# Kernel tuning notes

Hardware: AMD Instinct MI355X
Metric: run time of the kernel (lower is better)

The kernel has to match this reference:

```python
import jax, jax.numpy as jnp
import numpy as np

THETA = 10000.0
H, D_NOPE, D_ROPE, D_V = 12, 64, 64, 128
D_MODEL, D_LAT = 768, 128
B, S = 4, 2048


def _rope(x, pos, theta=THETA):
    # x: (B, S, D) with D even; pos: (S,) int. Matches RoPE.forward exactly
    # (interleaved even/odd rotation, freqs over full flattened D).
    D = x.shape[-1]
    inv_freq = 1.0 / theta ** (jnp.arange(0, D, 2, dtype=jnp.float32) / D)
    ang = pos.astype(jnp.float32)[:, None] * inv_freq        # (S, D/2)
    c, s = jnp.cos(ang), jnp.sin(ang)
    xe, xo = x[..., 0::2], x[..., 1::2]
    out = jnp.stack([xe * c - xo * s, xe * s + xo * c], axis=-1)
    return out.reshape(x.shape)


def setup_inputs() -> dict:
    key = jax.random.key(0)
    ks = jax.random.split(key, 12)
    std = 0.02
    inp = {
        'x': jax.random.normal(ks[0], (B, S, D_MODEL), jnp.float32),
        'token_positions': jnp.arange(S, dtype=jnp.int64) if jax.config.jax_enable_x64 else jnp.arange(S, dtype=jnp.int32),
        'W_dkv': jax.random.normal(ks[1], (D_LAT, D_MODEL), jnp.float32) * std,
        'b_dkv': jnp.zeros((D_LAT,), jnp.float32),
        'W_dq': jax.random.normal(ks[2], (D_LAT, D_MODEL), jnp.float32) * std,
        'b_dq': jnp.zeros((D_LAT,), jnp.float32),
        'W_uk_nope': jax.random.normal(ks[3], (H * D_NOPE, D_LAT), jnp.float32) * std,
        'b_uk_nope': jnp.zeros((H * D_NOPE,), jnp.float32),
        'W_uv': jax.random.normal(ks[4], (H * D_V, D_LAT), jnp.float32) * std,
        'b_uv': jnp.zeros((H * D_V,), jnp.float32),
        'W_uq_nope': jax.random.normal(ks[5], (H * D_NOPE, D_LAT), jnp.float32) * std,
        'b_uq_nope': jnp.zeros((H * D_NOPE,), jnp.float32),
        'W_uq_rope': jax.random.normal(ks[6], (H * D_ROPE, D_LAT), jnp.float32) * std,
        'b_uq_rope': jnp.zeros((H * D_ROPE,), jnp.float32),
        'W_uk_rope': jax.random.normal(ks[7], (H * D_ROPE, D_MODEL), jnp.float32) * std,
        'b_uk_rope': jnp.zeros((H * D_ROPE,), jnp.float32),
        'W_o': jax.random.normal(ks[8], (D_MODEL, H * D_V), jnp.float32) * std,
        'b_o': jnp.zeros((D_MODEL,), jnp.float32),
    }
    return inp


def reference(x, token_positions, W_dkv, b_dkv, W_dq, b_dq,
              W_uk_nope, b_uk_nope, W_uv, b_uv, W_uq_nope, b_uq_nope,
              W_uq_rope, b_uq_rope, W_uk_rope, b_uk_rope, W_o, b_o):
    b, s, _ = x.shape
    lin = lambda t, W, bb: t @ W.T + bb
    d_qk = D_NOPE + D_ROPE  # 128

    C_kv = lin(x, W_dkv, b_dkv)               # (B,S,128)
    C_q = lin(x, W_dq, b_dq)                  # (B,S,128)

    q_nope = lin(C_q, W_uq_nope, b_uq_nope)   # (B,S,H*64)
    k_nope = lin(C_kv, W_uk_nope, b_uk_nope)  # (B,S,H*64)
    v = lin(C_kv, W_uv, b_uv)                 # (B,S,H*128)

    q_rope = _rope(lin(C_q, W_uq_rope, b_uq_rope), token_positions)
    k_rope = _rope(lin(x, W_uk_rope, b_uk_rope), token_positions)

    # Faithful to torch: concat flattened nope||rope then view into heads.
    q = jnp.concatenate([q_nope, q_rope], axis=-1).reshape(b, s, H, d_qk).transpose(0, 2, 1, 3)
    k = jnp.concatenate([k_nope, k_rope], axis=-1).reshape(b, s, H, d_qk).transpose(0, 2, 1, 3)
    vh = v.reshape(b, s, H, D_V).transpose(0, 2, 1, 3)

    scale = 1.0 / jnp.sqrt(jnp.asarray(d_qk, x.dtype))
    logits = jnp.einsum('bhqd,bhkd->bhqk', q, k) * scale
    causal = jnp.tril(jnp.ones((s, s), bool))
    logits = jnp.where(causal, logits, jnp.finfo(logits.dtype).min)
    attn = jax.nn.softmax(logits, axis=-1)
    o = jnp.einsum('bhqk,bhkd->bhqd', attn, vh)      # (B,H,S,Dv)
    o = o.transpose(0, 2, 1, 3).reshape(b, s, H * D_V)
    return o @ W_o.T + b_o
```

## Files before the change

kernel.cpp:

```cpp
#include <hip/hip_runtime.h>

typedef __attribute__((ext_vector_type(8))) short short8;
typedef __attribute__((ext_vector_type(4))) short short4v;
typedef __attribute__((ext_vector_type(2))) int int2v;
typedef __attribute__((ext_vector_type(4))) float float4v;

#define MFMA16(a, b, c) __builtin_amdgcn_mfma_f32_16x16x32_bf16((a), (b), (c), 0, 0, 0)

__device__ __forceinline__ short f2bf(float f) {
  unsigned u = __float_as_uint(f);
  u += 0x7fffu + ((u >> 16) & 1u);
  return (short)(u >> 16);
}

__device__ __forceinline__ int cvtpk(float a, float b) {
  int r;
  asm("v_cvt_pk_bf16_f32 %0, %1, %2" : "=v"(r) : "v"(a), "v"(b));
  return r;
}

__device__ __forceinline__ void glds16(const short* g, short* l) {
  __builtin_amdgcn_global_load_lds(
      (const __attribute__((address_space(1))) void*)g,
      (__attribute__((address_space(3))) void*)l, 16, 0, 0);
}

struct CastSeg { const float* src; short* dst; int n4; };
struct CastArgs { CastSeg seg[9]; int start[10]; };

__global__ __launch_bounds__(256) void castk(CastArgs a) {
  int blk = blockIdx.x;
  int si = 0;
#pragma unroll
  for (int i = 1; i < 9; i++) si += (blk >= a.start[i]);
  int i = (blk - a.start[si]) * 256 + threadIdx.x;
  if (i >= a.seg[si].n4) return;
  float4v f = ((const float4v*)a.seg[si].src)[i];
  short4v o;
  o[0] = f2bf(f[0]); o[1] = f2bf(f[1]); o[2] = f2bf(f[2]); o[3] = f2bf(f[3]);
  ((short4v*)a.seg[si].dst)[i] = o;
}

struct GSeg {
  const short* A;
  const short* W;
  const float* bias0;
  const float* bias1;
  void* outp;
  int lda, ldw, bsplit, ropestart, ldo, ocol, K, flags;
};
struct GArgs { GSeg s[3]; int start[4]; };

__global__ __launch_bounds__(256, 2) void gemm_rt(GArgs ga, const int* __restrict__ pos) {
  int by = blockIdx.y;
  int si = (by >= ga.start[1]) + (by >= ga.start[2]);
  const GSeg sg = ga.s[si];
  int tid = threadIdx.x, w = tid >> 6, lane = tid & 63;
  int quad = lane >> 4, l16 = lane & 15;
  bool ropeF = sg.flags & 1, scaleF = sg.flags & 2;
  bool vtF = sg.flags & 4, f32F = sg.flags & 8, pairF = sg.flags & 16;
  int bm = blockIdx.x * 128;
  int bn = (by - ga.start[si]) * (pairF ? 256 : 128);
  int wm = (w & 1) * 64, wn = (w >> 1) * 64;
  int lda = sg.lda, ldw = sg.ldw;

  __shared__ short At[2][128 * 64];
  __shared__ short Bt[2][128 * 64];

  int srow[4], soff[4];
#pragma unroll
  for (int j = 0; j < 4; j++) {
    int r = w * 32 + j * 8 + (lane >> 3);
    srow[j] = r;
    soff[j] = ((lane & 7) ^ (r & 7)) << 3;
  }
  const short* Ag = sg.A + (size_t)bm * lda;
  const short* Wg = sg.W + (size_t)bn * ldw;

  float4v acc[4][4];
  float4v z = {0.f, 0.f, 0.f, 0.f};
#pragma unroll
  for (int mi = 0; mi < 4; mi++)
#pragma unroll
    for (int ni = 0; ni < 4; ni++) acc[mi][ni] = z;

  auto comp = [&](const short* Ab, const short* Bb) {
#pragma unroll
    for (int ks = 0; ks < 2; ks++) {
      short8 af[4], bf[4];
#pragma unroll
      for (int mi = 0; mi < 4; mi++) {
        int row = wm + mi * 16 + l16;
        af[mi] = *(const short8*)&Ab[(row << 6) + ((((ks << 2) + quad) ^ (row & 7)) << 3)];
      }
#pragma unroll
      for (int ni = 0; ni < 4; ni++) {
        int row = wn + ni * 16 + l16;
        bf[ni] = *(const short8*)&Bb[(row << 6) + ((((ks << 2) + quad) ^ (row & 7)) << 3)];
      }
#pragma unroll
      for (int mi = 0; mi < 4; mi++)
#pragma unroll
        for (int ni = 0; ni < 4; ni++)
          acc[mi][ni] = MFMA16(af[mi], bf[ni], acc[mi][ni]);
    }
  };

  auto epi = [&](int bnX) {
    if (vtF) {
      __syncthreads();
      short* T = &At[0][0];
#pragma unroll
      for (int ni = 0; ni < 4; ni++) {
        int col = wn + ni * 16 + l16;
        float bv = sg.bias0[bnX + col];
#pragma unroll
        for (int mi = 0; mi < 4; mi++) {
          int row0 = wm + mi * 16 + quad * 4;
          int rr = (row0 + ((col & 15) << 3)) & 127;
          short4v ov;
#pragma unroll
          for (int r = 0; r < 4; r++) ov[r] = f2bf(acc[mi][ni][r] + bv);
          *(short4v*)&T[col * 128 + rr] = ov;
        }
      }
      __syncthreads();
      int bidx = bm >> 11, s0 = bm & 2047;
      int sc = tid & 15;
#pragma unroll
      for (int cc = 0; cc < 8; cc++) {
        int c = cc * 16 + (tid >> 4);
        int rr = ((sc + (c & 15)) << 3) & 127;
        short8 v = *(const short8*)&T[c * 128 + rr];
        *(short8*)((short*)sg.outp + ((size_t)(bidx * 1536 + bnX + c)) * 2048 +
                   s0 + (sc << 3)) = v;
      }
      return;
    }
#pragma unroll
    for (int ni = 0; ni < 4; ni++) {
      int col = bnX + wn + ni * 16 + l16;
      float bv = (col < sg.bsplit) ? sg.bias0[col] : sg.bias1[col - sg.bsplit];
      float fr = 0.f;
      bool dorope = ropeF && (col >= sg.ropestart);
      if (dorope) {
        int ri = (col - sg.ropestart) & ~1;
        fr = exp2f((float)ri * (-13.287712379549449f / 768.0f));
      }
#pragma unroll
      for (int mi = 0; mi < 4; mi++) {
        int row0 = bm + wm + mi * 16 + quad * 4;
#pragma unroll
        for (int r = 0; r < 4; r++) {
          int row = row0 + r;
          float v = acc[mi][ni][r] + bv;
          if (ropeF) {
            float pv = __shfl_xor(v, 1, 64);
            if (dorope) {
              float ang = (float)pos[row & 2047] * fr;
              float sn, cs;
              __sincosf(ang, &sn, &cs);
              v = (col & 1) ? (pv * sn + v * cs) : (v * cs - pv * sn);
            }
          }
          if (scaleF) v *= 0.12751743f;
          if (f32F)
            ((float*)sg.outp)[(size_t)row * sg.ldo + sg.ocol + col] = v;
          else
            ((short*)sg.outp)[(size_t)row * sg.ldo + sg.ocol + col] = f2bf(v);
        }
      }
    }
  };

  int nk = sg.K >> 6;
  if (nk == 2) {
    auto stageB = [&](const short* Wg2) {
#pragma unroll
      for (int j = 0; j < 4; j++) {
        glds16(Wg2 + (size_t)srow[j] * ldw + soff[j], &Bt[0][(w * 32 + j * 8) * 64]);
        glds16(Wg2 + (size_t)srow[j] * ldw + 64 + soff[j], &Bt[1][(w * 32 + j * 8) * 64]);
      }
    };
#pragma unroll
    for (int j = 0; j < 4; j++) {
      glds16(Ag + (size_t)srow[j] * lda + soff[j], &At[0][(w * 32 + j * 8) * 64]);
      glds16(Ag + (size_t)srow[j] * lda + 64 + soff[j], &At[1][(w * 32 + j * 8) * 64]);
    }
    stageB(Wg);
    __syncthreads();
    comp(At[0], Bt[0]);
    comp(At[1], Bt[1]);
    if (pairF) {
      __syncthreads();
      stageB(Wg + (size_t)128 * ldw);
      epi(bn);
#pragma unroll
      for (int mi = 0; mi < 4; mi++)
#pragma unroll
        for (int ni = 0; ni < 4; ni++) acc[mi][ni] = z;
      __syncthreads();
      comp(At[0], Bt[0]);
      comp(At[1], Bt[1]);
      epi(bn + 128);
    } else {
      epi(bn);
    }
  } else {
#pragma unroll
    for (int j = 0; j < 4; j++)
      glds16(Ag + (size_t)srow[j] * lda + soff[j], &At[0][(w * 32 + j * 8) * 64]);
#pragma unroll
    for (int j = 0; j < 4; j++)
      glds16(Wg + (size_t)srow[j] * ldw + soff[j], &Bt[0][(w * 32 + j * 8) * 64]);
    for (int it = 0; it < nk; it++) {
      __syncthreads();
      if (it + 1 < nk) {
        int kt = (it + 1) << 6, nb = (it + 1) & 1;
#pragma unroll
        for (int j = 0; j < 4; j++)
          glds16(Ag + (size_t)srow[j] * lda + kt + soff[j],
                 &At[nb][(w * 32 + j * 8) * 64]);
#pragma unroll
        for (int j = 0; j < 4; j++)
          glds16(Wg + (size_t)srow[j] * ldw + kt + soff[j],
                 &Bt[nb][(w * 32 + j * 8) * 64]);
      }
      comp(At[it & 1], Bt[it & 1]);
    }
    epi(bn);
  }
}

__global__ __launch_bounds__(256, 2) void mla_attn(const short* __restrict__ Q,
                                                   const short* __restrict__ K,
                                                   const short* __restrict__ Vt,
                                                   short* __restrict__ O) {
  const int ld = 1536, SEQ = 2048;
  int tid = threadIdx.x, w = tid >> 6, lane = tid & 63;
  int quad = lane >> 4, l16 = lane & 15;
  int o = (int)blockIdx.x;
  int rank = o / 48;
  int g = o - rank * 48;
  int qt = (15 - rank) * 128;
  int hh = g % 12, b = g / 12;
  int qw = qt + w * 32;

  __shared__ short Kt[2][64 * 128];
  __shared__ short Vl[2][128 * 64];
  __shared__ short Pm[4][32 * 64];
  char* pwB = (char*)Pm[w];

  int kgo[4], vgo[4];
#pragma unroll
  for (int j = 0; j < 4; j++) {
    int rk = (w * 4 + j) * 4 + (lane >> 4);
    kgo[j] = rk * ld + (((lane & 15) ^ (rk & 7)) << 3);
    int rv = (w * 4 + j) * 8 + (lane >> 3);
    vgo[j] = rv * SEQ + (((lane & 7) ^ (rv & 7)) << 3);
  }
  const short* Kg = K + (size_t)b * SEQ * ld + hh * 128;
  const short* Vg = Vt + (size_t)(b * 12 + hh) * 128 * SEQ;

  short8 qf[2][4];
  {
    const short* Qg = Q + (size_t)(b * SEQ + qw + l16) * ld + hh * 128 + quad * 8;
#pragma unroll
    for (int nf = 0; nf < 2; nf++)
#pragma unroll
      for (int ks = 0; ks < 4; ks++)
        qf[nf][ks] = *(const short8*)(Qg + (size_t)nf * 16 * ld + ks * 32);
  }

  int koff[4][4], voff[2][8], pfo[2][2], pwo[2][4];
#pragma unroll
  for (int ks = 0; ks < 4; ks++)
#pragma unroll
    for (int mf = 0; mf < 4; mf++) {
      int row = mf * 16 + l16;
      koff[ks][mf] = row * 256 + ((((ks << 2) + quad) ^ (row & 7)) << 4);
    }
#pragma unroll
  for (int t = 0; t < 2; t++) {
#pragma unroll
    for (int df = 0; df < 8; df++) {
      int vr = df * 16 + l16;
      voff[t][df] = vr * 128 + ((((t << 2) + quad) ^ (vr & 7)) << 4);
    }
#pragma unroll
    for (int mq = 0; mq < 2; mq++)
      pfo[t][mq] = (mq * 16 + l16) * 128 + ((((t << 2) + quad) ^ (l16 & 7)) << 4);
#pragma unroll
    for (int mf = 0; mf < 4; mf++) {
      int p = (mf * 2 + (quad >> 1)) ^ (l16 & 7);
      pwo[t][mf] = (t * 16 + l16) * 128 + (p << 4) + ((quad & 1) << 3);
    }
  }

  float4v z = {0.f, 0.f, 0.f, 0.f};
  float4v oacc[2][8];
#pragma unroll
  for (int mq = 0; mq < 2; mq++)
#pragma unroll
    for (int df = 0; df < 8; df++) oacc[mq][df] = z;
  float l_i[2] = {0.f, 0.f};

#pragma unroll
  for (int j = 0; j < 4; j++) glds16(Kg + kgo[j], &Kt[0][(w * 4 + j) * 512]);
#pragma unroll
  for (int j = 0; j < 4; j++) glds16(Vg + vgo[j], &Vl[0][(w * 4 + j) * 512]);

  int ntiles = (qt >> 6) + 2;

#define ATTN_TILE(IT, NB, NB1)                                                 \
  do {                                                                         \
    int kt = (IT) << 6;                                                        \
    __syncthreads();                                                           \
    if ((IT) + 1 < ntiles) {                                                   \
      const short* kn = Kg + (size_t)(kt + 64) * ld;                           \
      const short* vn = Vg + (kt + 64);                                        \
      _Pragma("unroll") for (int j = 0; j < 4; j++)                            \
          glds16(kn + kgo[j], &Kt[NB1][(w * 4 + j) * 512]);                    \
      _Pragma("unroll") for (int j = 0; j < 4; j++)                            \
          glds16(vn + vgo[j], &Vl[NB1][(w * 4 + j) * 512]);                    \
    }                                                                          \
    if (kt <= qw + 31) {                                                       \
      const char* Kb = (const char*)Kt[NB];                                    \
      const char* Vb = (const char*)Vl[NB];                                    \
      float4v sf[4][2];                                                        \
      __builtin_amdgcn_s_setprio(1);                                           \
      _Pragma("unroll") for (int mf = 0; mf < 4; mf++) {                       \
        short8 a = *(const short8*)(Kb + koff[0][mf]);                         \
        sf[mf][0] = MFMA16(a, qf[0][0], z);                                    \
        sf[mf][1] = MFMA16(a, qf[1][0], z);                                    \
      }                                                                        \
      _Pragma("unroll") for (int ks = 1; ks < 4; ks++) {                       \
        _Pragma("unroll") for (int mf = 0; mf < 4; mf++) {                     \
          short8 a = *(const short8*)(Kb + koff[ks][mf]);                      \
          sf[mf][0] = MFMA16(a, qf[0][ks], sf[mf][0]);                         \
          sf[mf][1] = MFMA16(a, qf[1][ks], sf[mf][1]);                         \
        }                                                                      \
      }                                                                        \
      __builtin_amdgcn_s_setprio(0);                                           \
      if (kt + 63 > qw) {                                                      \
        _Pragma("unroll") for (int mf = 0; mf < 4; mf++) {                     \
          int key = kt + mf * 16 + quad * 4;                                   \
          _Pragma("unroll") for (int nf = 0; nf < 2; nf++) {                   \
            int q = qw + nf * 16 + l16;                                        \
            _Pragma("unroll") for (int r = 0; r < 4; r++)                      \
                if (key + r > q) sf[mf][nf][r] = -3e38f;                       \
          }                                                                    \
        }                                                                      \
      }                                                                        \
      _Pragma("unroll") for (int nf = 0; nf < 2; nf++) {                       \
        float ps = 0.f;                                                        \
        _Pragma("unroll") for (int mf = 0; mf < 4; mf++)                       \
            _Pragma("unroll") for (int r = 0; r < 4; r++) {                    \
          float e = exp2f(sf[mf][nf][r]);                                      \
          sf[mf][nf][r] = e;                                                   \
          ps += e;                                                             \
        }                                                                      \
        l_i[nf] += ps;                                                         \
        _Pragma("unroll") for (int mf = 0; mf < 4; mf++) {                     \
          int2v pk;                                                            \
          pk[0] = cvtpk(sf[mf][nf][0], sf[mf][nf][1]);                         \
          pk[1] = cvtpk(sf[mf][nf][2], sf[mf][nf][3]);                         \
          *(int2v*)(pwB + pwo[nf][mf]) = pk;                                   \
        }                                                                      \
      }                                                                        \
      __builtin_amdgcn_s_setprio(1);                                           \
      _Pragma("unroll") for (int t = 0; t < 2; t++) {                          \
        short8 pf0 = *(const short8*)(pwB + pfo[t][0]);                        \
        short8 pf1 = *(const short8*)(pwB + pfo[t][1]);                        \
        _Pragma("unroll") for (int df = 0; df < 8; df++) {                     \
          short8 vf = *(const short8*)(Vb + voff[t][df]);                      \
          oacc[0][df] = MFMA16(pf0, vf, oacc[0][df]);                          \
          oacc[1][df] = MFMA16(pf1, vf, oacc[1][df]);                          \
        }                                                                      \
      }                                                                        \
      __builtin_amdgcn_s_setprio(0);                                           \
    }                                                                          \
  } while (0)

  for (int it = 0; it < ntiles; it += 2) {
    ATTN_TILE(it, 0, 1);
    ATTN_TILE(it + 1, 1, 0);
  }
#undef ATTN_TILE

  short* Og = O + (size_t)(b * SEQ + qw) * ld + hh * 128;
#pragma unroll
  for (int mq = 0; mq < 2; mq++) {
    float l = l_i[mq];
    l += __shfl_xor(l, 16, 64);
    l += __shfl_xor(l, 32, 64);
    float linv = 1.0f / l;
    float lb[4];
#pragma unroll
    for (int r = 0; r < 4; r++) lb[r] = __shfl(linv, (quad << 2) + r, 64);
#pragma unroll
    for (int df = 0; df < 8; df++)
#pragma unroll
      for (int r = 0; r < 4; r++)
        Og[(size_t)(mq * 16 + (quad << 2) + r) * ld + df * 16 + l16] =
            f2bf(oacc[mq][df][r] * lb[r]);
  }
}

extern "C" void kernel_launch(void* const* d_in, const int* in_sizes, int n_in,
                              void* d_out, int out_size, void* d_ws, size_t ws_size,
                              hipStream_t stream) {
  const int S = 2048, DM = 768, DL = 128, HD = 1536;
  const int M = 4 * S;
  const int BIG = 1 << 28;

  const float* x = (const float*)d_in[0];
  const int* pos = (const int*)d_in[1];
  const float* W_dkv = (const float*)d_in[2];
  const float* b_dkv = (const float*)d_in[3];
  const float* W_dq = (const float*)d_in[4];
  const float* b_dq = (const float*)d_in[5];
  const float* W_uk_nope = (const float*)d_in[6];
  const float* b_uk_nope = (const float*)d_in[7];
  const float* W_uv = (const float*)d_in[8];
  const float* b_uv = (const float*)d_in[9];
  const float* W_uq_nope = (const float*)d_in[10];
  const float* b_uq_nope = (const float*)d_in[11];
  const float* W_uq_rope = (const float*)d_in[12];
  const float* b_uq_rope = (const float*)d_in[13];
  const float* W_uk_rope = (const float*)d_in[14];
  const float* b_uk_rope = (const float*)d_in[15];
  const float* W_o = (const float*)d_in[16];
  const float* b_o = (const float*)d_in[17];

  char* p = (char*)d_ws;
  size_t off = 0;
  auto take = [&](size_t nelem) -> short* {
    short* r = (short*)(p + off);
    off += (nelem * 2 + 255) & ~(size_t)255;
    return r;
  };
  short* xb = take((size_t)M * DM);
  short* Wdq = take(DL * DM);
  short* Wdkv = take(DL * DM);
  short* Wuqnope = take(768 * DL);
  short* Wuqrope = take(768 * DL);
  short* Wuknope = take(768 * DL);
  short* Wuv = take(1536 * DL);
  short* Wukrope = take(768 * DM);
  short* Wo = take(768 * 1536);
  short* Cm = take((size_t)M * 256);
  short* Qm = take((size_t)M * HD);
  short* Km = take((size_t)M * HD);
  short* Vtm = take((size_t)M * HD);
  short* Om = take((size_t)M * HD);
  if (off > ws_size) return;

  CastArgs ca;
  const float* srcs[9] = {x, W_dq, W_dkv, W_uq_nope, W_uq_rope, W_uk_nope, W_uv, W_uk_rope, W_o};
  short* dsts[9] = {xb, Wdq, Wdkv, Wuqnope, Wuqrope, Wuknope, Wuv, Wukrope, Wo};
  int ns[9] = {M * DM, DL * DM, DL * DM, 768 * DL, 768 * DL, 768 * DL, 1536 * DL, 768 * DM, 768 * 1536};
  ca.start[0] = 0;
  for (int i = 0; i < 9; i++) {
    ca.seg[i].src = srcs[i];
    ca.seg[i].dst = dsts[i];
    ca.seg[i].n4 = ns[i] / 4;
    ca.start[i + 1] = ca.start[i] + (ca.seg[i].n4 + 255) / 256;
  }
  castk<<<dim3(ca.start[9]), dim3(256), 0, stream>>>(ca);

  GArgs g1;
  g1.s[0].A = xb;   g1.s[0].W = Wdq;      g1.s[0].bias0 = b_dq;      g1.s[0].bias1 = b_dkv;
  g1.s[0].outp = Cm; g1.s[0].lda = DM; g1.s[0].ldw = DM; g1.s[0].bsplit = 128;
  g1.s[0].ropestart = 0; g1.s[0].ldo = 256; g1.s[0].ocol = 0; g1.s[0].K = DM; g1.s[0].flags = 0;
  g1.s[1].A = xb;   g1.s[1].W = Wukrope;  g1.s[1].bias0 = b_uk_rope; g1.s[1].bias1 = b_uk_rope;
  g1.s[1].outp = Km; g1.s[1].lda = DM; g1.s[1].ldw = DM; g1.s[1].bsplit = BIG;
  g1.s[1].ropestart = 0; g1.s[1].ldo = HD; g1.s[1].ocol = 768; g1.s[1].K = DM; g1.s[1].flags = 1;
  g1.s[2] = g1.s[1];
  g1.start[0] = 0; g1.start[1] = 2; g1.start[2] = 8; g1.start[3] = 8;
  gemm_rt<<<dim3(M / 128, 8), dim3(256), 0, stream>>>(g1, pos);

  GArgs g2;
  g2.s[0].A = Cm;   g2.s[0].W = Wuqnope;  g2.s[0].bias0 = b_uq_nope; g2.s[0].bias1 = b_uq_rope;
  g2.s[0].outp = Qm; g2.s[0].lda = 256; g2.s[0].ldw = DL; g2.s[0].bsplit = 768;
  g2.s[0].ropestart = 768; g2.s[0].ldo = HD; g2.s[0].ocol = 0; g2.s[0].K = DL;
  g2.s[0].flags = 1 | 2 | 16;
  g2.s[1].A = Cm + 128; g2.s[1].W = Wuknope; g2.s[1].bias0 = b_uk_nope; g2.s[1].bias1 = b_uk_nope;
  g2.s[1].outp = Km; g2.s[1].lda = 256; g2.s[1].ldw = DL; g2.s[1].bsplit = BIG;
  g2.s[1].ropestart = 0; g2.s[1].ldo = HD; g2.s[1].ocol = 0; g2.s[1].K = DL;
  g2.s[1].flags = 16;
  g2.s[2].A = Cm + 128; g2.s[2].W = Wuv;   g2.s[2].bias0 = b_uv;      g2.s[2].bias1 = b_uv;
  g2.s[2].outp = Vtm; g2.s[2].lda = 256; g2.s[2].ldw = DL; g2.s[2].bsplit = BIG;
  g2.s[2].ropestart = 0; g2.s[2].ldo = 0; g2.s[2].ocol = 0; g2.s[2].K = DL;
  g2.s[2].flags = 4;
  g2.start[0] = 0; g2.start[1] = 6; g2.start[2] = 9; g2.start[3] = 21;
  gemm_rt<<<dim3(M / 128, 21), dim3(256), 0, stream>>>(g2, pos);

  mla_attn<<<dim3(768), dim3(256), 0, stream>>>(Qm, Km, Vtm, Om);

  GArgs g3;
  g3.s[0].A = Om;   g3.s[0].W = Wo;       g3.s[0].bias0 = b_o;       g3.s[0].bias1 = b_o;
  g3.s[0].outp = d_out; g3.s[0].lda = HD; g3.s[0].ldw = HD; g3.s[0].bsplit = BIG;
  g3.s[0].ropestart = 0; g3.s[0].ldo = 768; g3.s[0].ocol = 0; g3.s[0].K = HD; g3.s[0].flags = 8;
  g3.s[1] = g3.s[0];
  g3.s[2] = g3.s[0];
  g3.start[0] = 0; g3.start[1] = 6; g3.start[2] = 6; g3.start[3] = 6;
  gemm_rt<<<dim3(M / 128, 6), dim3(256), 0, stream>>>(g3, pos);
}
```

Baseline: 304.3 us.

## Halve attention KV tile to 32 keys and raise occupancy to 4 blocks/CU

The attention kernel now streams keys and values in 32-key tiles instead of 64. It shrinks the K, V and P shared-memory buffers, rewrites the swizzle offsets and causal-tile bookkeeping to match, and raises launch bounds to 4 waves-per-EU blocks. The goal is higher occupancy and less shared memory and register use per block, so more waves can hide latency. The cost is twice as many barriers and global-load issues per key range, with less MFMA work between syncs. The GEMM kernel is also templated per launch with a tag, which gives separate instantiations but no real code difference.

```diff
diff --git a/kernel.cpp b/kernel.cpp
--- a/kernel.cpp
+++ b/kernel.cpp
@@ -51,6 +51,7 @@
 };
 struct GArgs { GSeg s[3]; int start[4]; };
 
+template <int TAG>
 __global__ __launch_bounds__(256, 2) void gemm_rt(GArgs ga, const int* __restrict__ pos) {
   int by = blockIdx.y;
   int si = (by >= ga.start[1]) + (by >= ga.start[2]);
@@ -232,7 +233,7 @@
   }
 }
 
-__global__ __launch_bounds__(256, 2) void mla_attn(const short* __restrict__ Q,
+__global__ __launch_bounds__(256, 4) void mla_attn(const short* __restrict__ Q,
                                                    const short* __restrict__ K,
                                                    const short* __restrict__ Vt,
                                                    short* __restrict__ O) {
@@ -246,18 +247,18 @@
   int hh = g % 12, b = g / 12;
   int qw = qt + w * 32;
 
-  __shared__ short Kt[2][64 * 128];
-  __shared__ short Vl[2][128 * 64];
-  __shared__ short Pm[4][32 * 64];
+  __shared__ short Kt[2][32 * 128];
+  __shared__ short Vl[2][128 * 32];
+  __shared__ short Pm[4][32 * 32];
   char* pwB = (char*)Pm[w];
 
-  int kgo[4], vgo[4];
-#pragma unroll
-  for (int j = 0; j < 4; j++) {
-    int rk = (w * 4 + j) * 4 + (lane >> 4);
-    kgo[j] = rk * ld + (((lane & 15) ^ (rk & 7)) << 3);
-    int rv = (w * 4 + j) * 8 + (lane >> 3);
-    vgo[j] = rv * SEQ + (((lane & 7) ^ (rv & 7)) << 3);
+  int kgo[2], vgo[2];
+#pragma unroll
+  for (int j = 0; j < 2; j++) {
+    int rk = w * 8 + j * 4 + quad;
+    kgo[j] = rk * ld + ((l16 ^ (rk & 7)) << 3);
+    int rv = j * 64 + w * 16 + (lane >> 2);
+    vgo[j] = rv * SEQ + (((lane & 3) ^ (rv & 3)) << 3);
   }
   const short* Kg = K + (size_t)b * SEQ * ld + hh * 128;
   const short* Vg = Vt + (size_t)(b * 12 + hh) * 128 * SEQ;
@@ -272,30 +273,28 @@
         qf[nf][ks] = *(const short8*)(Qg + (size_t)nf * 16 * ld + ks * 32);
   }
 
-  int koff[4][4], voff[2][8], pfo[2][2], pwo[2][4];
+  int koff[4][2], voff[8], pfo[2], pwo[2][2];
 #pragma unroll
   for (int ks = 0; ks < 4; ks++)
 #pragma unroll
-    for (int mf = 0; mf < 4; mf++) {
+    for (int mf = 0; mf < 2; mf++) {
       int row = mf * 16 + l16;
       koff[ks][mf] = row * 256 + ((((ks << 2) + quad) ^ (row & 7)) << 4);
     }
 #pragma unroll
-  for (int t = 0; t < 2; t++) {
-#pragma unroll
-    for (int df = 0; df < 8; df++) {
-      int vr = df * 16 + l16;
-      voff[t][df] = vr * 128 + ((((t << 2) + quad) ^ (vr & 7)) << 4);
-    }
-#pragma unroll
-    for (int mq = 0; mq < 2; mq++)
-      pfo[t][mq] = (mq * 16 + l16) * 128 + ((((t << 2) + quad) ^ (l16 & 7)) << 4);
-#pragma unroll
-    for (int mf = 0; mf < 4; mf++) {
-      int p = (mf * 2 + (quad >> 1)) ^ (l16 & 7);
-      pwo[t][mf] = (t * 16 + l16) * 128 + (p << 4) + ((quad & 1) << 3);
-    }
-  }
+  for (int df = 0; df < 8; df++) {
+    int vr = df * 16 + l16;
+    voff[df] = vr * 64 + ((quad ^ (vr & 3)) << 4);
+  }
+#pragma unroll
+  for (int mq = 0; mq < 2; mq++)
+    pfo[mq] = (mq * 16 + l16) * 64 + ((quad ^ (l16 & 3)) << 4);
+#pragma unroll
+  for (int nf = 0; nf < 2; nf++)
+#pragma unroll
+    for (int mf = 0; mf < 2; mf++)
+      pwo[nf][mf] = (nf * 16 + l16) * 64 +
+                    (((mf * 2 + (quad >> 1)) ^ (l16 & 3)) << 4) + ((quad & 1) << 3);
 
   float4v z = {0.f, 0.f, 0.f, 0.f};
   float4v oacc[2][8];
@@ -306,44 +305,44 @@
   float l_i[2] = {0.f, 0.f};
 
 #pragma unroll
-  for (int j = 0; j < 4; j++) glds16(Kg + kgo[j], &Kt[0][(w * 4 + j) * 512]);
-#pragma unroll
-  for (int j = 0; j < 4; j++) glds16(Vg + vgo[j], &Vl[0][(w * 4 + j) * 512]);
-
-  int ntiles = (qt >> 6) + 2;
+  for (int j = 0; j < 2; j++) glds16(Kg + kgo[j], &Kt[0][(w * 8 + j * 4) * 128]);
+#pragma unroll
+  for (int j = 0; j < 2; j++) glds16(Vg + vgo[j], &Vl[0][(j * 64 + w * 16) * 32]);
+
+  int ntiles = (qt >> 5) + 4;
 
 #define ATTN_TILE(IT, NB, NB1)                                                 \
   do {                                                                         \
-    int kt = (IT) << 6;                                                        \
+    int kt = (IT) << 5;                                                        \
     __syncthreads();                                                           \
     if ((IT) + 1 < ntiles) {                                                   \
-      const short* kn = Kg + (size_t)(kt + 64) * ld;                           \
-      const short* vn = Vg + (kt + 64);                                        \
-      _Pragma("unroll") for (int j = 0; j < 4; j++)                            \
-          glds16(kn + kgo[j], &Kt[NB1][(w * 4 + j) * 512]);                    \
-      _Pragma("unroll") for (int j = 0; j < 4; j++)                            \
-          glds16(vn + vgo[j], &Vl[NB1][(w * 4 + j) * 512]);                    \
+      const short* kn = Kg + (size_t)(kt + 32) * ld;                           \
+      const short* vn = Vg + (kt + 32);                                        \
+      _Pragma("unroll") for (int j = 0; j < 2; j++)                            \
+          glds16(kn + kgo[j], &Kt[NB1][(w * 8 + j * 4) * 128]);                \
+      _Pragma("unroll") for (int j = 0; j < 2; j++)                            \
+          glds16(vn + vgo[j], &Vl[NB1][(j * 64 + w * 16) * 32]);               \
     }                                                                          \
     if (kt <= qw + 31) {                                                       \
       const char* Kb = (const char*)Kt[NB];                                    \
       const char* Vb = (const char*)Vl[NB];                                    \
-      float4v sf[4][2];                                                        \
+      float4v sf[2][2];                                                        \
       __builtin_amdgcn_s_setprio(1);                                           \
-      _Pragma("unroll") for (int mf = 0; mf < 4; mf++) {                       \
+      _Pragma("unroll") for (int mf = 0; mf < 2; mf++) {                       \
         short8 a = *(const short8*)(Kb + koff[0][mf]);                         \
         sf[mf][0] = MFMA16(a, qf[0][0], z);                                    \
         sf[mf][1] = MFMA16(a, qf[1][0], z);                                    \
       }                                                                        \
       _Pragma("unroll") for (int ks = 1; ks < 4; ks++) {                       \
-        _Pragma("unroll") for (int mf = 0; mf < 4; mf++) {                     \
+        _Pragma("unroll") for (int mf = 0; mf < 2; mf++) {                     \
           short8 a = *(const short8*)(Kb + koff[ks][mf]);                      \
           sf[mf][0] = MFMA16(a, qf[0][ks], sf[mf][0]);                         \
           sf[mf][1] = MFMA16(a, qf[1][ks], sf[mf][1]);                         \
         }                                                                      \
       }                                                                        \
       __builtin_amdgcn_s_setprio(0);                                           \
-      if (kt + 63 > qw) {                                                      \
-        _Pragma("unroll") for (int mf = 0; mf < 4; mf++) {                     \
+      if (kt + 31 > qw) {                                                      \
+        _Pragma("unroll") for (int mf = 0; mf < 2; mf++) {                     \
           int key = kt + mf * 16 + quad * 4;                                   \
           _Pragma("unroll") for (int nf = 0; nf < 2; nf++) {                   \
             int q = qw + nf * 16 + l16;                                        \
@@ -354,14 +353,14 @@
       }                                                                        \
       _Pragma("unroll") for (int nf = 0; nf < 2; nf++) {                       \
         float ps = 0.f;                                                        \
-        _Pragma("unroll") for (int mf = 0; mf < 4; mf++)                       \
+        _Pragma("unroll") for (int mf = 0; mf < 2; mf++)                       \
             _Pragma("unroll") for (int r = 0; r < 4; r++) {                    \
           float e = exp2f(sf[mf][nf][r]);                                      \
           sf[mf][nf][r] = e;                                                   \
           ps += e;                                                             \
         }                                                                      \
         l_i[nf] += ps;                                                         \
-        _Pragma("unroll") for (int mf = 0; mf < 4; mf++) {                     \
+        _Pragma("unroll") for (int mf = 0; mf < 2; mf++) {                     \
           int2v pk;                                                            \
           pk[0] = cvtpk(sf[mf][nf][0], sf[mf][nf][1]);                         \
           pk[1] = cvtpk(sf[mf][nf][2], sf[mf][nf][3]);                         \
@@ -369,11 +368,11 @@
         }                                                                      \
       }                                                                        \
       __builtin_amdgcn_s_setprio(1);                                           \
-      _Pragma("unroll") for (int t = 0; t < 2; t++) {                          \
-        short8 pf0 = *(const short8*)(pwB + pfo[t][0]);                        \
-        short8 pf1 = *(const short8*)(pwB + pfo[t][1]);                        \
+      {                                                                        \
+        short8 pf0 = *(const short8*)(pwB + pfo[0]);                           \
+        short8 pf1 = *(const short8*)(pwB + pfo[1]);                           \
         _Pragma("unroll") for (int df = 0; df < 8; df++) {                     \
-          short8 vf = *(const short8*)(Vb + voff[t][df]);                      \
+          short8 vf = *(const short8*)(Vb + voff[df]);                         \
           oacc[0][df] = MFMA16(pf0, vf, oacc[0][df]);                          \
           oacc[1][df] = MFMA16(pf1, vf, oacc[1][df]);                          \
         }                                                                      \
@@ -478,7 +477,7 @@
   g1.s[1].ropestart = 0; g1.s[1].ldo = HD; g1.s[1].ocol = 768; g1.s[1].K = DM; g1.s[1].flags = 1;
   g1.s[2] = g1.s[1];
   g1.start[0] = 0; g1.start[1] = 2; g1.start[2] = 8; g1.start[3] = 8;
-  gemm_rt<<<dim3(M / 128, 8), dim3(256), 0, stream>>>(g1, pos);
+  gemm_rt<1><<<dim3(M / 128, 8), dim3(256), 0, stream>>>(g1, pos);
 
   GArgs g2;
   g2.s[0].A = Cm;   g2.s[0].W = Wuqnope;  g2.s[0].bias0 = b_uq_nope; g2.s[0].bias1 = b_uq_rope;
@@ -494,7 +493,7 @@
   g2.s[2].ropestart = 0; g2.s[2].ldo = 0; g2.s[2].ocol = 0; g2.s[2].K = DL;
   g2.s[2].flags = 4;
   g2.start[0] = 0; g2.start[1] = 6; g2.start[2] = 9; g2.start[3] = 21;
-  gemm_rt<<<dim3(M / 128, 21), dim3(256), 0, stream>>>(g2, pos);
+  gemm_rt<2><<<dim3(M / 128, 21), dim3(256), 0, stream>>>(g2, pos);
 
   mla_attn<<<dim3(768), dim3(256), 0, stream>>>(Qm, Km, Vtm, Om);
 
@@ -505,5 +504,5 @@
   g3.s[1] = g3.s[0];
   g3.s[2] = g3.s[0];
   g3.start[0] = 0; g3.start[1] = 6; g3.start[2] = 6; g3.start[3] = 6;
-  gemm_rt<<<dim3(M / 128, 6), dim3(256), 0, stream>>>(g3, pos);
-}
+  gemm_rt<3><<<dim3(M / 128, 6), dim3(256), 0, stream>>>(g3, pos);
+}
```

After: 409.4 us. 1.35x slower.
